# Optimization experiments

Measured on AMD Instinct MI355X. Metric: run time of the kernel, lower is better.

The kernel has to match this reference:

```python
import jax, jax.numpy as jnp
from jax import lax
import numpy as np

H = 512       # nhidden
IN = 300      # title/body input dim
TLEN = 40     # title_len
BLEN = 200    # body_len
B = 256       # batch
CH = 512      # classify_hidden
NC = 4        # nclass


def setup_inputs():
    key = jax.random.key(0)
    ks = jax.random.split(key, 17)
    s = 1.0 / np.sqrt(H)
    u = lambda k, sh: jax.random.uniform(k, sh, jnp.float32, -s, s)
    return {
        "x": jax.random.normal(ks[0], (B, TLEN + BLEN, IN), jnp.float32),
        "title_Wih": u(ks[1], (2, 4 * H, IN)),
        "title_Whh": u(ks[2], (2, 4 * H, H)),
        "title_bih": u(ks[3], (2, 4 * H)),
        "title_bhh": u(ks[4], (2, 4 * H)),
        "body_Wih": u(ks[5], (2, 4 * H, IN)),
        "body_Whh": u(ks[6], (2, 4 * H, H)),
        "body_bih": u(ks[7], (2, 4 * H)),
        "body_bhh": u(ks[8], (2, 4 * H)),
        "bil_W": u(ks[9], (1, 2 * H, 2 * H)),
        "bil_b": u(ks[10], (1,)),
        "attn_W": u(ks[11], (2 * H, 4 * H)),
        "attn_b": u(ks[12], (2 * H,)),
        "dec_W": u(ks[13], (CH, 4 * H)),
        "dec_b": u(ks[14], (CH,)),
        "cls_W": u(ks[15], (NC, CH)),
        "cls_b": u(ks[16], (NC,)),
    }


def _lstm_dir(x, Wih, Whh, bih, bhh, h0, c0, reverse):
    # x: [B, T, I]; precompute input-to-gate contributions for all timesteps
    xg = jnp.einsum('bti,gi->btg', x, Wih) + bih + bhh  # [B, T, 4H]

    def step(carry, xg_t):
        h, c = carry
        g = xg_t + h @ Whh.T  # PyTorch gate order: i, f, g, o
        i, f, gg, o = jnp.split(g, 4, axis=-1)
        c = jax.nn.sigmoid(f) * c + jax.nn.sigmoid(i) * jnp.tanh(gg)
        h = jax.nn.sigmoid(o) * jnp.tanh(c)
        return (h, c), h

    (hT, cT), hs = lax.scan(step, (h0, c0), jnp.swapaxes(xg, 0, 1), reverse=reverse)
    return jnp.swapaxes(hs, 0, 1), hT, cT  # outputs aligned to input time order


def _bilstm(x, Wih, Whh, bih, bhh, h0, c0):
    # h0, c0: [2, B, H] (dir 0 = forward, dir 1 = backward)
    out_f, hf, cf = _lstm_dir(x, Wih[0], Whh[0], bih[0], bhh[0], h0[0], c0[0], False)
    out_b, hb, cb = _lstm_dir(x, Wih[1], Whh[1], bih[1], bhh[1], h0[1], c0[1], True)
    out = jnp.concatenate([out_f, out_b], axis=-1)  # [B, T, 2H]
    return out, jnp.stack([hf, hb]), jnp.stack([cf, cb])


def reference(x, title_Wih, title_Whh, title_bih, title_bhh,
              body_Wih, body_Whh, body_bih, body_bhh,
              bil_W, bil_b, attn_W, attn_b, dec_W, dec_b, cls_W, cls_b):
    title, body = x[:, :TLEN, :], x[:, TLEN:, :]
    z = jnp.zeros((2, x.shape[0], H), x.dtype)
    title_out, hn, cn = _bilstm(title, title_Wih, title_Whh, title_bih, title_bhh, z, z)
    # conditional=True: body RNN starts from title final (h, c)
    body_out, _, _ = _bilstm(body, body_Wih, body_Whh, body_bih, body_bhh, hn, cn)
    body_last = body_out[:, -1, :]  # [B, 2H]
    # vectorized bilinear attention over title timesteps (replaces per-t loop)
    scores = jnp.einsum('bte,oeh,bh->bto', title_out, bil_W, body_last) + bil_b
    scores = jax.nn.softmax(scores[..., 0], axis=-1)  # [B, TLEN]
    context = jnp.einsum('bte,bt->be', title_out, scores)  # [B, 2H]
    attn = jnp.tanh(jnp.concatenate([context, body_last], axis=1) @ attn_W.T + attn_b)
    output = jnp.concatenate([title_out[:, -1, :], attn], axis=1)  # [B, 4H]
    class_hidden = output @ dec_W.T + dec_b  # dropout p=0.0 -> identity
    return jax.nn.softmax(class_hidden @ cls_W.T + cls_b, axis=-1)
```

## Files before the change

### kernel.cpp

```cpp
#include <hip/hip_runtime.h>
#include <math.h>

#define HD    512
#define BATCH 256
#define TDIM  240
#define INDIM 300

typedef unsigned short u16;
typedef u16   u16x8 __attribute__((ext_vector_type(8)));
typedef float f32x4 __attribute__((ext_vector_type(4)));

__device__ __forceinline__ u16 bf16_rte(float v) {
    unsigned u = __builtin_bit_cast(unsigned, v);
    unsigned r = (u + 0x7FFFu + ((u >> 16) & 1u)) >> 16;
    return (u16)r;
}

__device__ __forceinline__ void mfma16(f32x4& d, u16x8 a, u16x8 b) {
    asm("v_mfma_f32_16x16x32_bf16 %0, %1, %2, %0" : "+v"(d) : "v"(a), "v"(b));
}

__global__ __launch_bounds__(256) void split_pad(
    const float* __restrict__ src, u16* __restrict__ hi, u16* __restrict__ lo,
    int rows, int kin, int kout)
// ... 4 lines not shown
    int k = (int)(i - (long)r * kout);
    float v = (k < kin) ? src[(long)r * kin + k] : 0.f;
    u16 h = bf16_rte(v);
    float hf = __builtin_bit_cast(float, (unsigned)h << 16);
    hi[i] = h;
    lo[i] = bf16_rte(v - hf);
}

struct SJob { const float* src; u16* hi; u16* lo; int kin; int kout; };
struct SParams { SJob j[12]; long cum[13]; };

__global__ __launch_bounds__(256) void split_all(SParams P)
{
    long gid = (long)blockIdx.x * 256 + threadIdx.x;
    if (gid >= P.cum[12]) return;
    int sgi = 0;
    #pragma unroll
    for (int k = 1; k < 12; ++k) if (gid >= P.cum[k]) sgi = k;
    const SJob& J = P.j[sgi];
    long i = gid - P.cum[sgi];
    int r = (int)(i / J.kout);
    int k = (int)(i - (long)r * J.kout);
    float v = (k < J.kin) ? J.src[(long)r * J.kin + k] : 0.f;
    u16 h = bf16_rte(v);
    float hf = __builtin_bit_cast(float, (unsigned)h << 16);
    J.hi[i] = h;
    J.lo[i] = bf16_rte(v - hf);
}

struct StepDir {
    const u16* Wih_h; const u16* Wih_l;
    const u16* Whh_h; const u16* Whh_l;
    const float* bih; const float* bhh;
    const u16* hh; const u16* hl;
    u16* oh; u16* ol;
    float* c;
    float* ex; long exs;
    int t;
};

__global__ __launch_bounds__(64) void step_mfma(
    const u16* __restrict__ xh, const u16* __restrict__ xl,
    StepDir d0, StepDir d1)
{
    StepDir D = blockIdx.z ? d1 : d0;
    const int gx   = blockIdx.x;
    const int xcd  = gx & 7, j = gx >> 3;
    const int cblk = xcd * 4 + (j & 3);
    const int rblk = j >> 2;
    const int lane = threadIdx.x;
    const int lr   = lane & 15;
    const int lk8  = (lane >> 4) * 8;
    const int b0   = rblk * 32;
    const int col  = cblk * 16 + lr;

    f32x4 acc[2][4];
    #pragma unroll
    for (int g = 0; g < 4; ++g) {
        float bs = D.bih[g * HD + col] + D.bhh[g * HD + col];
        acc[0][g] = f32x4{bs, bs, bs, bs};
        acc[1][g] = f32x4{bs, bs, bs, bs};
    }

    u16x8 Ah0[2], Al0[2], Bh0[4], Bl0[4];
    u16x8 Ah1[2], Al1[2], Bh1[4], Bl1[4];

    auto MMA = [&](u16x8 (&Ah)[2], u16x8 (&Al)[2], u16x8 (&Bh)[4], u16x8 (&Bl)[4]) {
        #pragma unroll
        for (int rt = 0; rt < 2; ++rt)
            #pragma unroll
            for (int g = 0; g < 4; ++g) {
                mfma16(acc[rt][g], Ah[rt], Bh[g]);
                mfma16(acc[rt][g], Ah[rt], Bl[g]);
                mfma16(acc[rt][g], Al[rt], Bh[g]);
            }
    };

    {
        auto LD = [&](u16x8 (&Ah)[2], u16x8 (&Al)[2], u16x8 (&Bh)[4], u16x8 (&Bl)[4], int ks) {
            const int ko = ks * 32 + lk8;
            #pragma unroll
            for (int rt = 0; rt < 2; ++rt) {
                long off = ((long)(b0 + rt * 16 + lr) * TDIM + D.t) * 320 + ko;
                Ah[rt] = *(const u16x8*)(xh + off);
                Al[rt] = *(const u16x8*)(xl + off);
            }
            #pragma unroll
            for (int g = 0; g < 4; ++g) {
                long off = (long)(g * HD + col) * 320 + ko;
                Bh[g] = *(const u16x8*)(D.Wih_h + off);
                Bl[g] = *(const u16x8*)(D.Wih_l + off);
            }
        };
        LD(Ah0, Al0, Bh0, Bl0, 0);
        #pragma unroll
        for (int ks = 0; ks < 10; ks += 2) {
            LD(Ah1, Al1, Bh1, Bl1, ks + 1);
            MMA(Ah0, Al0, Bh0, Bl0);
            if (ks + 2 < 10) LD(Ah0, Al0, Bh0, Bl0, ks + 2);
            MMA(Ah1, Al1, Bh1, Bl1);
        }
    }
    {
        auto LD = [&](u16x8 (&Ah)[2], u16x8 (&Al)[2], u16x8 (&Bh)[4], u16x8 (&Bl)[4], int ks) {
            const int ko = ks * 32 + lk8;
            #pragma unroll
            for (int rt = 0; rt < 2; ++rt) {
                long off = (long)(b0 + rt * 16 + lr) * HD + ko;
                Ah[rt] = *(const u16x8*)(D.hh + off);
                Al[rt] = *(const u16x8*)(D.hl + off);
            }
            #pragma unroll
            for (int g = 0; g < 4; ++g) {
                long off = (long)(g * HD + col) * HD + ko;
                Bh[g] = *(const u16x8*)(D.Whh_h + off);
                Bl[g] = *(const u16x8*)(D.Whh_l + off);
            }
        };
        LD(Ah0, Al0, Bh0, Bl0, 0);
        #pragma unroll
        for (int ks = 0; ks < 16; ks += 2) {
            LD(Ah1, Al1, Bh1, Bl1, ks + 1);
            MMA(Ah0, Al0, Bh0, Bl0);
            if (ks + 2 < 16) LD(Ah0, Al0, Bh0, Bl0, ks + 2);
            MMA(Ah1, Al1, Bh1, Bl1);
        }
    }

    #pragma unroll
    for (int rt = 0; rt < 2; ++rt) {
        #pragma unroll
        for (int r = 0; r < 4; ++r) {
            const int b = b0 + rt * 16 + (lane >> 4) * 4 + r;
            const long hoff = (long)b * HD + col;
            float iv = acc[rt][0][r];
            float fv = acc[rt][1][r];
            float gv = acc[rt][2][r];
            float ov = acc[rt][3][r];
            float cp = D.c[hoff];
            float si = 1.f / (1.f + expf(-iv));
            float sf = 1.f / (1.f + expf(-fv));
            float so = 1.f / (1.f + expf(-ov));
            float cn = sf * cp + si * tanhf(gv);
            float hn = so * tanhf(cn);
            D.c[hoff] = cn;
            u16 hb = bf16_rte(hn);
            D.oh[hoff] = hb;
            D.ol[hoff] = bf16_rte(hn - __builtin_bit_cast(float, (unsigned)hb << 16));
            if (D.ex) D.ex[(long)b * D.exs + col] = hn;
        }
    }
}

__global__ __launch_bounds__(64) void xg_mfma(
    const u16* __restrict__ xh, const u16* __restrict__ xl,
    const u16* __restrict__ Wih_h, const u16* __restrict__ Wih_l,
    const float* __restrict__ bih, const float* __restrict__ bhh,
    float* __restrict__ xgT, int t0abs, int tstep)
{
    const int bx   = blockIdx.x;
    const int tloc = bx >> 9;
    const int rem  = bx & 511;
    const int rblk = rem >> 6;
    const int cgrp = rem & 63;
    const int lane = threadIdx.x;
    const int lr = lane & 15, lk8 = (lane >> 4) * 8;
    const int b0 = rblk * 32;
    const int tx = t0abs + tstep * tloc;
    const int colf0 = cgrp * 32 + lr;
    const int colf1 = colf0 + 16;

    f32x4 acc[2][2];
    {
        float bs0 = bih[colf0] + bhh[colf0];
        float bs1 = bih[colf1] + bhh[colf1];
        acc[0][0] = f32x4{bs0, bs0, bs0, bs0};
        acc[1][0] = f32x4{bs0, bs0, bs0, bs0};
        acc[0][1] = f32x4{bs1, bs1, bs1, bs1};
        acc[1][1] = f32x4{bs1, bs1, bs1, bs1};
    }

    u16x8 a0h[2], a0l[2], b0h[2], b0l[2];
    u16x8 a1h[2], a1l[2], b1h[2], b1l[2];

    auto LD = [&](u16x8 (&Ah)[2], u16x8 (&Al)[2], u16x8 (&Bh)[2], u16x8 (&Bl)[2], int ks) {
        const int ko = ks * 32 + lk8;
        #pragma unroll
        for (int rt = 0; rt < 2; ++rt) {
            long off = ((long)(b0 + rt * 16 + lr) * TDIM + tx) * 320 + ko;
            Ah[rt] = *(const u16x8*)(xh + off);
            Al[rt] = *(const u16x8*)(xl + off);
        }
        long w0 = (long)colf0 * 320 + ko;
        long w1 = (long)colf1 * 320 + ko;
        Bh[0] = *(const u16x8*)(Wih_h + w0);
        Bl[0] = *(const u16x8*)(Wih_l + w0);
        Bh[1] = *(const u16x8*)(Wih_h + w1);
        Bl[1] = *(const u16x8*)(Wih_l + w1);
    };
    auto MMA = [&](u16x8 (&Ah)[2], u16x8 (&Al)[2], u16x8 (&Bh)[2], u16x8 (&Bl)[2]) {
        #pragma unroll
        for (int rt = 0; rt < 2; ++rt)
            #pragma unroll
            for (int cf = 0; cf < 2; ++cf) {
                mfma16(acc[rt][cf], Ah[rt], Bh[cf]);
                mfma16(acc[rt][cf], Ah[rt], Bl[cf]);
                mfma16(acc[rt][cf], Al[rt], Bh[cf]);
            }
    };

    LD(a0h, a0l, b0h, b0l, 0);
    #pragma unroll
    for (int ks = 0; ks < 10; ks += 2) {
        LD(a1h, a1l, b1h, b1l, ks + 1);
        MMA(a0h, a0l, b0h, b0l);
        if (ks + 2 < 10) LD(a0h, a0l, b0h, b0l, ks + 2);
        MMA(a1h, a1l, b1h, b1l);
    }

    #pragma unroll
    for (int rt = 0; rt < 2; ++rt) {
        long o0 = ((long)tloc * 2048 + colf0) * 256 + b0 + rt * 16 + (lane >> 4) * 4;
        long o1 = ((long)tloc * 2048 + colf1) * 256 + b0 + rt * 16 + (lane >> 4) * 4;
        *(f32x4*)(xgT + o0) = acc[rt][0];
        *(f32x4*)(xgT + o1) = acc[rt][1];
    }
}

__device__ __forceinline__ void group_bar(unsigned* cnt, unsigned* gen,
                                          unsigned nb, unsigned g)
{
    __syncthreads();
    if (threadIdx.x == 0) {
        unsigned old = __hip_atomic_fetch_add(cnt, 1u, __ATOMIC_RELEASE,
                                              __HIP_MEMORY_SCOPE_AGENT);
        if (old == nb - 1u) {
            __hip_atomic_store(cnt, 0u, __ATOMIC_RELAXED, __HIP_MEMORY_SCOPE_AGENT);
            __hip_atomic_store(gen, g + 1u, __ATOMIC_RELEASE, __HIP_MEMORY_SCOPE_AGENT);
        } else {
            while (__hip_atomic_load(gen, __ATOMIC_RELAXED, __HIP_MEMORY_SCOPE_AGENT) < g + 1u)
                __builtin_amdgcn_s_sleep(2);
            (void)__hip_atomic_load(gen, __ATOMIC_ACQUIRE, __HIP_MEMORY_SCOPE_AGENT);
        }
    }
    __syncthreads();
}

__global__ __launch_bounds__(256) void lstm_persist(
    const float* __restrict__ xgT,
    const u16* __restrict__ Whh_h, const u16* __restrict__ Whh_l,
    u16* __restrict__ hAh, u16* __restrict__ hAl,
    u16* __restrict__ hBh, u16* __restrict__ hBl,
    float* __restrict__ cst,
    float* __restrict__ ex, long ex_bstride, int ex_t0, int ex_tstep,
    int ex_coff, int ex_final,
    unsigned* __restrict__ bars, int s0, int L)
{
    const int gx   = blockIdx.x;
    const int rblk = gx & 7;
    const int cblk = gx >> 3;
    const int wid  = threadIdx.x >> 6;
    const int lane = threadIdx.x & 63;
    const int lr   = lane & 15;
    const int lk8  = (lane >> 4) * 8;
    const int b0   = rblk * 32;
    const int col  = cblk * 16 + lr;

    __shared__ u16 WH[64][520];
    __shared__ u16 WL[64][520];
    __shared__ f32x4 RED[3][64][8];

    for (int idx = threadIdx.x; idx < 64 * 64; idx += 256) {
        int rr = idx >> 6;
        int kk = (idx & 63) << 3;
        int g = rr >> 4, cc = rr & 15;
        long gro = (long)(g * HD + cblk * 16 + cc) * HD + kk;
        *(u16x8*)&WH[rr][kk] = *(const u16x8*)(Whh_h + gro);
        *(u16x8*)&WL[rr][kk] = *(const u16x8*)(Whh_l + gro);
    }
    __syncthreads();

    unsigned* bcnt = bars + rblk * 64;
    unsigned* bgen = bars + 512 + rblk * 64;
    unsigned gen = 0;
    const int ksbase = wid * 4;

    for (int ti = 0; ti < L; ++ti) {
        const int s = s0 + ti;
        const u16* hih = (s & 1) ? hBh : hAh;
        const u16* hil = (s & 1) ? hBl : hAl;
        u16* hoh = (s & 1) ? hAh : hBh;
        u16* hol = (s & 1) ? hAl : hBl;

        f32x4 acc[2][4];
        if (wid == 0) {
            #pragma unroll
            for (int rt = 0; rt < 2; ++rt)
                #pragma unroll
                for (int g = 0; g < 4; ++g) {
                    long o = ((long)ti * 2048 + g * HD + col) * 256
                             + b0 + rt * 16 + (lane >> 4) * 4;
                    acc[rt][g] = __builtin_nontemporal_load((const f32x4*)(xgT + o));
                }
        } else {
            #pragma unroll
            for (int rt = 0; rt < 2; ++rt)
                #pragma unroll
                for (int g = 0; g < 4; ++g) acc[rt][g] = f32x4{0.f, 0.f, 0.f, 0.f};
        }

        u16x8 Ah0[2], Al0[2], Bh0[4], Bl0[4];
        u16x8 Ah1[2], Al1[2], Bh1[4], Bl1[4];

        auto MMA = [&](u16x8 (&Ah)[2], u16x8 (&Al)[2], u16x8 (&Bh)[4], u16x8 (&Bl)[4]) {
            #pragma unroll
            for (int rt = 0; rt < 2; ++rt)
                #pragma unroll
                for (int g = 0; g < 4; ++g) {
                    mfma16(acc[rt][g], Ah[rt], Bh[g]);
                    mfma16(acc[rt][g], Ah[rt], Bl[g]);
                    mfma16(acc[rt][g], Al[rt], Bh[g]);
                }
        };
        auto LD = [&](u16x8 (&Ah)[2], u16x8 (&Al)[2], u16x8 (&Bh)[4], u16x8 (&Bl)[4], int ks) {
            const int ko = ks * 32 + lk8;
            #pragma unroll
            for (int rt = 0; rt < 2; ++rt) {
                long off = (long)(b0 + rt * 16 + lr) * HD + ko;
                Ah[rt] = *(const u16x8*)(hih + off);
                Al[rt] = *(const u16x8*)(hil + off);
            }
            #pragma unroll
            for (int g = 0; g < 4; ++g) {
                Bh[g] = *(const u16x8*)&WH[g * 16 + lr][ko];
                Bl[g] = *(const u16x8*)&WL[g * 16 + lr][ko];
            }
        };

        LD(Ah0, Al0, Bh0, Bl0, ksbase + 0);
        LD(Ah1, Al1, Bh1, Bl1, ksbase + 1);
        MMA(Ah0, Al0, Bh0, Bl0);
        LD(Ah0, Al0, Bh0, Bl0, ksbase + 2);
        MMA(Ah1, Al1, Bh1, Bl1);
        LD(Ah1, Al1, Bh1, Bl1, ksbase + 3);
        MMA(Ah0, Al0, Bh0, Bl0);
        MMA(Ah1, Al1, Bh1, Bl1);

        if (wid != 0) {
            #pragma unroll
            for (int rt = 0; rt < 2; ++rt)
                #pragma unroll
                for (int g = 0; g < 4; ++g)
                    RED[wid - 1][lane][rt * 4 + g] = acc[rt][g];
        }
        __syncthreads();

        if (wid == 0) {
            #pragma unroll
            for (int w = 0; w < 3; ++w)
                #pragma unroll
                for (int rt = 0; rt < 2; ++rt)
                    #pragma unroll
                    for (int g = 0; g < 4; ++g)
                        acc[rt][g] += RED[w][lane][rt * 4 + g];

            const bool exw = (ex_final == -2) || (ex_final >= 0 && ti == ex_final);
            const int tt = ex_t0 + ex_tstep * ti;
            #pragma unroll
            for (int rt = 0; rt < 2; ++rt) {
                #pragma unroll
                for (int r = 0; r < 4; ++r) {
                    const int b = b0 + rt * 16 + (lane >> 4) * 4 + r;
                    const long hoff = (long)b * HD + col;
                    float iv = acc[rt][0][r];
                    float fv = acc[rt][1][r];
                    float gv = acc[rt][2][r];
                    float ov = acc[rt][3][r];
                    float cp = cst[hoff];
                    float si = 1.f / (1.f + expf(-iv));
                    float sf = 1.f / (1.f + expf(-fv));
                    float so = 1.f / (1.f + expf(-ov));
                    float cn = sf * cp + si * tanhf(gv);
                    float hn = so * tanhf(cn);
                    cst[hoff] = cn;
                    u16 hb = bf16_rte(hn);
                    hoh[hoff] = hb;
                    hol[hoff] = bf16_rte(hn - __builtin_bit_cast(float, (unsigned)hb << 16));
                    if (exw) ex[(long)b * ex_bstride + (long)tt * 1024 + ex_coff + col] = hn;
                }
            }
        }
        if (ti + 1 < L) { group_bar(bcnt, bgen, 32u, gen); ++gen; }
    }
}

struct DualDir {
    const u16* Whh_h; const u16* Whh_l;
    u16 *hAh, *hAl, *hBh, *hBl;
    float* cst;
    float* ex; long exb; int ext0, extstep, excoff;
};

__global__ __launch_bounds__(256) void lstm_persist_dual(
    const float* __restrict__ xgT, long dirStride,
    DualDir d0, DualDir d1,
    unsigned* __restrict__ bars, int s0, int L)
{
    const int gx   = blockIdx.x;
    const int grp  = gx & 7;
    const int dir  = grp >> 2;
    const int rb2  = grp & 3;
    const int cblk = gx >> 3;
    const int wid  = threadIdx.x >> 6;
    const int lane = threadIdx.x & 63;
    const int lr   = lane & 15;
    const int lk8  = (lane >> 4) * 8;
    const int col  = cblk * 16 + lr;

    const DualDir D = dir ? d1 : d0;
    const float* xgD = xgT + (dir ? dirStride : 0);

    __shared__ u16 WH[64][520];
    __shared__ u16 WL[64][520];
    __shared__ f32x4 RED[3][64][8];

    for (int idx = threadIdx.x; idx < 64 * 64; idx += 256) {
        int rr = idx >> 6;
        int kk = (idx & 63) << 3;
        int g = rr >> 4, cc = rr & 15;
        long gro = (long)(g * HD + cblk * 16 + cc) * HD + kk;
        *(u16x8*)&WH[rr][kk] = *(const u16x8*)(D.Whh_h + gro);
        *(u16x8*)&WL[rr][kk] = *(const u16x8*)(D.Whh_l + gro);
    }
    __syncthreads();

    unsigned* bcnt = bars + grp * 64;
    unsigned* bgen = bars + 512 + grp * 64;
    unsigned gen = 0;
    const int ksbase = wid * 4;

    for (int ti = 0; ti < L; ++ti) {
        const int s = s0 + ti;
        const u16* hih = (s & 1) ? D.hBh : D.hAh;
        const u16* hil = (s & 1) ? D.hBl : D.hAl;
        u16* hoh = (s & 1) ? D.hAh : D.hBh;
        u16* hol = (s & 1) ? D.hAl : D.hBl;

        #pragma unroll
        for (int t2 = 0; t2 < 2; ++t2) {
            const int b0 = rb2 * 64 + t2 * 32;

            f32x4 acc[2][4];
            if (wid == 0) {
                #pragma unroll
                for (int rt = 0; rt < 2; ++rt)
                    #pragma unroll
                    for (int g = 0; g < 4; ++g) {
                        long o = ((long)ti * 2048 + g * HD + col) * 256
                                 + b0 + rt * 16 + (lane >> 4) * 4;
                        acc[rt][g] = __builtin_nontemporal_load((const f32x4*)(xgD + o));
                    }
            } else {
                #pragma unroll
                for (int rt = 0; rt < 2; ++rt)
                    #pragma unroll
                    for (int g = 0; g < 4; ++g) acc[rt][g] = f32x4{0.f, 0.f, 0.f, 0.f};
            }

            u16x8 Ah0[2], Al0[2], Bh0[4], Bl0[4];
            u16x8 Ah1[2], Al1[2], Bh1[4], Bl1[4];

            auto MMA = [&](u16x8 (&Ah)[2], u16x8 (&Al)[2], u16x8 (&Bh)[4], u16x8 (&Bl)[4]) {
                #pragma unroll
                for (int rt = 0; rt < 2; ++rt)
                    #pragma unroll
                    for (int g = 0; g < 4; ++g) {
                        mfma16(acc[rt][g], Ah[rt], Bh[g]);
                        mfma16(acc[rt][g], Ah[rt], Bl[g]);
                        mfma16(acc[rt][g], Al[rt], Bh[g]);
                    }
            };
            auto LD = [&](u16x8 (&Ah)[2], u16x8 (&Al)[2], u16x8 (&Bh)[4], u16x8 (&Bl)[4], int ks) {
                const int ko = ks * 32 + lk8;
                #pragma unroll
                for (int rt = 0; rt < 2; ++rt) {
                    long off = (long)(b0 + rt * 16 + lr) * HD + ko;
                    Ah[rt] = *(const u16x8*)(hih + off);
                    Al[rt] = *(const u16x8*)(hil + off);
                }
                #pragma unroll
                for (int g = 0; g < 4; ++g) {
                    Bh[g] = *(const u16x8*)&WH[g * 16 + lr][ko];
                    Bl[g] = *(const u16x8*)&WL[g * 16 + lr][ko];
                }
            };

            LD(Ah0, Al0, Bh0, Bl0, ksbase + 0);
            LD(Ah1, Al1, Bh1, Bl1, ksbase + 1);
            MMA(Ah0, Al0, Bh0, Bl0);
            LD(Ah0, Al0, Bh0, Bl0, ksbase + 2);
            MMA(Ah1, Al1, Bh1, Bl1);
            LD(Ah1, Al1, Bh1, Bl1, ksbase + 3);
            MMA(Ah0, Al0, Bh0, Bl0);
            MMA(Ah1, Al1, Bh1, Bl1);

            if (wid != 0) {
                #pragma unroll
                for (int rt = 0; rt < 2; ++rt)
                    #pragma unroll
                    for (int g = 0; g < 4; ++g)
                        RED[wid - 1][lane][rt * 4 + g] = acc[rt][g];
            }
            __syncthreads();

            if (wid == 0) {
                #pragma unroll
                for (int w = 0; w < 3; ++w)
                    #pragma unroll
                    for (int rt = 0; rt < 2; ++rt)
                        #pragma unroll
                        for (int g = 0; g < 4; ++g)
                            acc[rt][g] += RED[w][lane][rt * 4 + g];

                const int tt = D.ext0 + D.extstep * ti;
                #pragma unroll
                for (int rt = 0; rt < 2; ++rt) {
                    #pragma unroll
                    for (int r = 0; r < 4; ++r) {
                        const int b = b0 + rt * 16 + (lane >> 4) * 4 + r;
                        const long hoff = (long)b * HD + col;
                        float iv = acc[rt][0][r];
                        float fv = acc[rt][1][r];
                        float gv = acc[rt][2][r];
                        float ov = acc[rt][3][r];
                        float cp = D.cst[hoff];
                        float si = 1.f / (1.f + expf(-iv));
                        float sf = 1.f / (1.f + expf(-fv));
                        float so = 1.f / (1.f + expf(-ov));
                        float cn = sf * cp + si * tanhf(gv);
                        float hn = so * tanhf(cn);
                        D.cst[hoff] = cn;
                        u16 hb = bf16_rte(hn);
                        hoh[hoff] = hb;
                        hol[hoff] = bf16_rte(hn - __builtin_bit_cast(float, (unsigned)hb << 16));
                        D.ex[(long)b * D.exb + (long)tt * 1024 + D.excoff + col] = hn;
                    }
                }
            }
            __syncthreads();
        }
        if (ti + 1 < L) { group_bar(bcnt, bgen, 32u, gen); ++gen; }
    }
}

__global__ __launch_bounds__(64) void body_persist(
    const u16* __restrict__ xh, const u16* __restrict__ xl,
    const u16* __restrict__ Wih_h, const u16* __restrict__ Wih_l,
    const u16* __restrict__ Whh_h, const u16* __restrict__ Whh_l,
    const float* __restrict__ bih, const float* __restrict__ bhh,
    u16* __restrict__ hAh, u16* __restrict__ hAl,
    u16* __restrict__ hBh, u16* __restrict__ hBl,
// ... 353 lines not shown
        }
        __syncthreads();
    }
    #pragma unroll
    for (int r = 0; r < 2; ++r) {
        int m = mblk*32 + ty*2 + r;
        #pragma unroll
        for (int q = 0; q < 4; ++q) {
            int n = nblk*64 + q*16 + txd;
            float v = acc[r][q] + (bias ? bias[n] : 0.f);
            if (ACT == 1) v = tanhf(v);
            C[m*ldc + n] = v;
        }
    }
}

__global__ __launch_bounds__(256) void attn_ctx(
    const float* __restrict__ title_out,
    const float* __restrict__ u,
    const float* __restrict__ bilb,
    float* __restrict__ attn_in)
{
    int b = blockIdx.x;
    int tid = threadIdx.x;
    __shared__ float uL[1024];
    __shared__ float sc[40];
    for (int e = tid; e < 1024; e += 256) uL[e] = u[b*1024 + e];
    __syncthreads();
    int wave = tid >> 6, lane = tid & 63;
    for (int t = wave*10; t < wave*10 + 10; ++t) {
        const float* row = title_out + (b*40 + t)*1024;
        float s = 0.f;
        for (int e = lane; e < 1024; e += 64) s += row[e]*uL[e];
        #pragma unroll
        for (int off = 32; off > 0; off >>= 1) s += __shfl_down(s, off, 64);
        if (lane == 0) sc[t] = s + bilb[0];
    }
    __syncthreads();
    if (tid < 64) {
        float v = (tid < 40) ? sc[tid] : -1e30f;
        float m = v;
        #pragma unroll
        for (int off = 32; off > 0; off >>= 1) m = fmaxf(m, __shfl_xor(m, off, 64));
        float e = (tid < 40) ? expf(v - m) : 0.f;
        float ssum = e;
        #pragma unroll
        for (int off = 32; off > 0; off >>= 1) ssum += __shfl_xor(ssum, off, 64);
        if (tid < 40) sc[tid] = e / ssum;
    }
    __syncthreads();
    for (int e = tid; e < 1024; e += 256) {
        float a = 0.f;
        #pragma unroll
        for (int t = 0; t < 40; ++t) a += sc[t]*title_out[(b*40 + t)*1024 + e];
        attn_in[b*2048 + e] = a;
    }
}

__global__ void copy_rows(const float* __restrict__ src, int ss,
                          float* __restrict__ dst, int ds, int n)
{
    int b = blockIdx.x;
    for (int e = threadIdx.x; e < n; e += blockDim.x) dst[b*ds + e] = src[b*ss + e];
}

__global__ __launch_bounds__(64) void final_cls(
    const float* __restrict__ ch,
    const float* __restrict__ clsW,
    const float* __restrict__ clsb,
    float* __restrict__ out)
{
    int b = blockIdx.x*64 + threadIdx.x;
    float o[4];
    #pragma unroll
    for (int n = 0; n < 4; ++n) {
        float s = clsb[n];
        for (int jj = 0; jj < 512; ++jj) s += ch[b*512 + jj]*clsW[n*512 + jj];
        o[n] = s;
    }
    float m = fmaxf(fmaxf(o[0], o[1]), fmaxf(o[2], o[3]));
    float e0 = expf(o[0]-m), e1 = expf(o[1]-m), e2 = expf(o[2]-m), e3 = expf(o[3]-m);
    float s = e0 + e1 + e2 + e3;
    out[b*4+0] = e0/s; out[b*4+1] = e1/s; out[b*4+2] = e2/s; out[b*4+3] = e3/s;
}

extern "C" void kernel_launch(void* const* d_in, const int* in_sizes, int n_in,
                              void* d_out, int out_size, void* d_ws, size_t ws_size,
                              hipStream_t stream) {
    const float* x     = (const float*)d_in[0];
    const float* tWih  = (const float*)d_in[1];
    const float* tWhh  = (const float*)d_in[2];
    const float* tbih  = (const float*)d_in[3];
    const float* tbhh  = (const float*)d_in[4];
    const float* bWih  = (const float*)d_in[5];
    const float* bWhh  = (const float*)d_in[6];
    const float* bbih  = (const float*)d_in[7];
    const float* bbhh  = (const float*)d_in[8];
    const float* bilW  = (const float*)d_in[9];
    const float* bilb  = (const float*)d_in[10];
    const float* attnW = (const float*)d_in[11];
    const float* attnb = (const float*)d_in[12];
    const float* decW  = (const float*)d_in[13];
    const float* decb  = (const float*)d_in[14];
    const float* clsW  = (const float*)d_in[15];
    const float* clsb  = (const float*)d_in[16];

    char* base = (char*)d_ws;
    size_t off = 0;
    auto carve = [&](size_t bytes) -> void* {
        void* r = base + off; off += (bytes + 255) & ~(size_t)255; return r;
    };

    u16* hA0h = (u16*)carve(BATCH*HD*2);
    u16* hA0l = (u16*)carve(BATCH*HD*2);
    u16* hA1h = (u16*)carve(BATCH*HD*2);
    u16* hA1l = (u16*)carve(BATCH*HD*2);
    float* c0 = (float*)carve(BATCH*HD*4);
    float* c1 = (float*)carve(BATCH*HD*4);
    unsigned* bars = (unsigned*)carve(32*4096);
    size_t zero_bytes = off;
    u16* hB0h = (u16*)carve(BATCH*HD*2);
    u16* hB0l = (u16*)carve(BATCH*HD*2);
    u16* hB1h = (u16*)carve(BATCH*HD*2);
    u16* hB1l = (u16*)carve(BATCH*HD*2);
    u16* xh = (u16*)carve((size_t)BATCH*TDIM*320*2);
    u16* xl = (u16*)carve((size_t)BATCH*TDIM*320*2);
    u16* tW0ih_h = (u16*)carve(2048*320*2); u16* tW0ih_l = (u16*)carve(2048*320*2);
    u16* tW1ih_h = (u16*)carve(2048*320*2); u16* tW1ih_l = (u16*)carve(2048*320*2);
    u16* bW0ih_h = (u16*)carve(2048*320*2); u16* bW0ih_l = (u16*)carve(2048*320*2);
    u16* bW1ih_h = (u16*)carve(2048*320*2); u16* bW1ih_l = (u16*)carve(2048*320*2);
    u16* tW0hh_h = (u16*)carve(2048*512*2); u16* tW0hh_l = (u16*)carve(2048*512*2);
    u16* tW1hh_h = (u16*)carve(2048*512*2); u16* tW1hh_l = (u16*)carve(2048*512*2);
    u16* bW0hh_h = (u16*)carve(2048*512*2); u16* bW0hh_l = (u16*)carve(2048*512*2);
    u16* bW1hh_h = (u16*)carve(2048*512*2); u16* bW1hh_l = (u16*)carve(2048*512*2);
    float* title_out = (float*)carve((size_t)BATCH*40*1024*4);
    float* body_last = (float*)carve((size_t)BATCH*1024*4);
    float* u_buf     = (float*)carve((size_t)BATCH*1024*4);
    float* attn_in   = (float*)carve((size_t)BATCH*2048*4);
    float* out_cat   = (float*)carve((size_t)BATCH*2048*4);
    float* ch        = (float*)carve((size_t)BATCH*512*4);
    u16* bl_h = (u16*)carve((size_t)BATCH*1024*2); u16* bl_l = (u16*)carve((size_t)BATCH*1024*2);
    u16* ai_h = (u16*)carve((size_t)BATCH*2048*2); u16* ai_l = (u16*)carve((size_t)BATCH*2048*2);
    u16* oc_h = (u16*)carve((size_t)BATCH*2048*2); u16* oc_l = (u16*)carve((size_t)BATCH*2048*2);
    u16* bilW_h  = (u16*)carve(1024*1024*2); u16* bilW_l  = (u16*)carve(1024*1024*2);
    u16* attnW_h = (u16*)carve((size_t)1024*2048*2); u16* attnW_l = (u16*)carve((size_t)1024*2048*2);
    u16* decW_h  = (u16*)carve((size_t)512*2048*2);  u16* decW_l  = (u16*)carve((size_t)512*2048*2);
    size_t need = off;

    const size_t SLAB_BYTES = (size_t)2048 * 256 * 4;
    const long   SLABF = 2048L * 256;
    float* xgT = (float*)(base + off);
    size_t nslab = 0;
    if (ws_size > need) nslab = (ws_size - need) / SLAB_BYTES;
    int C = (int)(nslab > 50 ? 50 : nslab);
    const bool xg_ok = (C >= 10);
    int C2 = (int)(nslab / 2 > 40 ? 40 : nslab / 2);
    const bool dual_ok = (C2 >= 10);

    if (ws_size >= need) {
        hipMemsetAsync(d_ws, 0, zero_bytes, stream);

        {
            SParams P;
            auto J = [&](int i, const float* s, u16* h, u16* l, long rows, int kin, int kout) {
                P.j[i] = { s, h, l, kin, kout };
                P.cum[i + 1] = P.cum[i] + rows * (long)kout;
            };
            P.cum[0] = 0;
            J(0,  x,                  xh,      xl,      (long)BATCH*TDIM, INDIM, 320);
            J(1,  tWih,               tW0ih_h, tW0ih_l, 2048, INDIM, 320);
            J(2,  tWih + 2048*INDIM,  tW1ih_h, tW1ih_l, 2048, INDIM, 320);
            J(3,  bWih,               bW0ih_h, bW0ih_l, 2048, INDIM, 320);
            J(4,  bWih + 2048*INDIM,  bW1ih_h, bW1ih_l, 2048, INDIM, 320);
            J(5,  tWhh,               tW0hh_h, tW0hh_l, 2048, HD, HD);
            J(6,  tWhh + 2048*HD,     tW1hh_h, tW1hh_l, 2048, HD, HD);
            J(7,  bWhh,               bW0hh_h, bW0hh_l, 2048, HD, HD);
            J(8,  bWhh + 2048*HD,     bW1hh_h, bW1hh_l, 2048, HD, HD);
            J(9,  bilW,               bilW_h,  bilW_l,  1024, 1024, 1024);
            J(10, attnW,              attnW_h, attnW_l, 1024, 2048, 2048);
            J(11, decW,               decW_h,  decW_l,  512,  2048, 2048);
            long total = P.cum[12];
            split_all<<<dim3((unsigned)((total + 255) / 256)), 256, 0, stream>>>(P);
        }

        if (xg_ok) {
            int ci = 0;
            if (dual_ok) {
                for (int tb = 0; tb < 40; tb += C2, ++ci) {
                    int L = (C2 < 40 - tb) ? C2 : (40 - tb);
                    xg_mfma<<<dim3((unsigned)(L*512)), 64, 0, stream>>>(
                        xh, xl, tW0ih_h, tW0ih_l, tbih, tbhh, xgT, tb, 1);
                    xg_mfma<<<dim3((unsigned)(L*512)), 64, 0, stream>>>(
                        xh, xl, tW1ih_h, tW1ih_l, tbih + 2048, tbhh + 2048,
                        xgT + (long)L * SLABF, 39 - tb, -1);
                    DualDir D0 = { tW0hh_h, tW0hh_l, hA0h, hA0l, hB0h, hB0l, c0,
                                   title_out, 40*1024, tb, 1, 0 };
                    DualDir D1 = { tW1hh_h, tW1hh_l, hA1h, hA1l, hB1h, hB1l, c1,
                                   title_out, 40*1024, 39 - tb, -1, 512 };
                    lstm_persist_dual<<<dim3(256), 256, 0, stream>>>(
                        xgT, (long)L * SLABF, D0, D1,
                        bars + (size_t)ci*1024, tb, L);
                }
            } else {
                for (int tb = 0; tb < 40; tb += C, ++ci) {
                    int L = (C < 40 - tb) ? C : (40 - tb);
                    xg_mfma<<<dim3((unsigned)(L*512)), 64, 0, stream>>>(
                        xh, xl, tW0ih_h, tW0ih_l, tbih, tbhh, xgT, tb, 1);
                    lstm_persist<<<dim3(256), 256, 0, stream>>>(
                        xgT, tW0hh_h, tW0hh_l, hA0h, hA0l, hB0h, hB0l, c0,
                        title_out, 40*1024, tb, 1, 0, -2,
                        bars + (size_t)ci*1024, tb, L);
                }
                for (int tb = 0; tb < 40; tb += C, ++ci) {
                    int L = (C < 40 - tb) ? C : (40 - tb);
                    xg_mfma<<<dim3((unsigned)(L*512)), 64, 0, stream>>>(
                        xh, xl, tW1ih_h, tW1ih_l, tbih + 2048, tbhh + 2048, xgT, 39 - tb, -1);
                    lstm_persist<<<dim3(256), 256, 0, stream>>>(
                        xgT, tW1hh_h, tW1hh_l, hA1h, hA1l, hB1h, hB1l, c1,
                        title_out, 40*1024, 39 - tb, -1, 512, -2,
                        bars + (size_t)ci*1024, tb, L);
                }
            }
            {
                StepDir F = { bW0ih_h, bW0ih_l, bW0hh_h, bW0hh_l, bbih, bbhh,
                              hA0h, hA0l, hB0h, hB0l, c0, (float*)nullptr, 0, 40 };
                StepDir R = { bW1ih_h, bW1ih_l, bW1hh_h, bW1hh_l, bbih + 2048, bbhh + 2048,
                              hA1h, hA1l, hB1h, hB1l, c1, body_last + 512, 1024, 239 };
                step_mfma<<<dim3(256,1,2), 64, 0, stream>>>(xh, xl, F, R);
            }
            for (int tb = 1; tb < 200; tb += C, ++ci) {
                int L = (C < 200 - tb) ? C : (200 - tb);
                bool last = (tb + L == 200);
                xg_mfma<<<dim3((unsigned)(L*512)), 64, 0, stream>>>(
                    xh, xl, bW0ih_h, bW0ih_l, bbih, bbhh, xgT, 40 + tb, 1);
                lstm_persist<<<dim3(256), 256, 0, stream>>>(
                    xgT, bW0hh_h, bW0hh_l, hA0h, hA0l, hB0h, hB0l, c0,
                    body_last, 1024, 0, 0, 0, last ? (L - 1) : -1,
                    bars + (size_t)ci*1024, 40 + tb, L);
            }
        } else {
            for (int t = 0; t < 40; ++t) {
                bool odd = t & 1;
                StepDir A = { tW0ih_h, tW0ih_l, tW0hh_h, tW0hh_l, tbih, tbhh,
                              odd?hB0h:hA0h, odd?hB0l:hA0l, odd?hA0h:hB0h, odd?hA0l:hB0l,
                              c0, title_out + (size_t)t*1024, 40*1024, t };
                StepDir B = { tW1ih_h, tW1ih_l, tW1hh_h, tW1hh_l, tbih + 2048, tbhh + 2048,
                              odd?hB1h:hA1h, odd?hB1l:hA1l, odd?hA1h:hB1h, odd?hA1l:hB1l,
                              c1, title_out + (size_t)(39 - t)*1024 + 512, 40*1024, 39 - t };
                step_mfma<<<dim3(256,1,2), 64, 0, stream>>>(xh, xl, A, B);
            }
            {
                StepDir F = { bW0ih_h, bW0ih_l, bW0hh_h, bW0hh_l, bbih, bbhh,
                              hA0h, hA0l, hB0h, hB0l, c0, (float*)nullptr, 0, 40 };
                StepDir R = { bW1ih_h, bW1ih_l, bW1hh_h, bW1hh_l, bbih + 2048, bbhh + 2048,
                              hA1h, hA1l, hB1h, hB1l, c1, body_last + 512, 1024, 239 };
                step_mfma<<<dim3(256,1,2), 64, 0, stream>>>(xh, xl, F, R);
            }
            body_persist<<<dim3(256), 64, 0, stream>>>(
                xh, xl, bW0ih_h, bW0ih_l, bW0hh_h, bW0hh_l, bbih, bbhh,
                hA0h, hA0l, hB0h, hB0l, c0, body_last, bars);
        }

        split_pad<<<dim3((unsigned)((256*1024 + 255)/256)), 256, 0, stream>>>(
            body_last, bl_h, bl_l, 256, 1024, 1024);
        mfma_gemm<0><<<dim3(8*64), 64, 0, stream>>>(bl_h, bl_l, bilW_h, bilW_l,
                                                    (const float*)nullptr, u_buf, 1024, 1024, 64);
        attn_ctx<<<256, 256, 0, stream>>>(title_out, u_buf, bilb, attn_in);
        copy_rows<<<256, 256, 0, stream>>>(body_last, 1024, attn_in + 1024, 2048, 1024);
        copy_rows<<<256, 256, 0, stream>>>(title_out + 39*1024, 40*1024, out_cat, 2048, 1024);
        split_pad<<<dim3((unsigned)((256*2048 + 255)/256)), 256, 0, stream>>>(
            attn_in, ai_h, ai_l, 256, 2048, 2048);
        mfma_gemm<1><<<dim3(8*64), 64, 0, stream>>>(ai_h, ai_l, attnW_h, attnW_l,
                                                    attnb, out_cat + 1024, 2048, 2048, 64);
        split_pad<<<dim3((unsigned)((256*2048 + 255)/256)), 256, 0, stream>>>(
            out_cat, oc_h, oc_l, 256, 2048, 2048);
        mfma_gemm<0><<<dim3(8*32), 64, 0, stream>>>(oc_h, oc_l, decW_h, decW_l,
                                                    decb, ch, 512, 2048, 32);
        final_cls<<<4, 64, 0, stream>>>(ch, clsW, clsb, (float*)d_out);
    } else {
        float* p = (float*)d_ws;
        float* lhA0 = p; p += BATCH*HD;
        float* lc0  = p; p += BATCH*HD;
        float* lhA1 = p; p += BATCH*HD;
        float* lc1  = p; p += BATCH*HD;
        float* lhB0 = p; p += BATCH*HD;
        float* lhB1 = p; p += BATCH*HD;
        float* l_title = p; p += (size_t)BATCH*40*1024;
        float* l_blast = p; p += BATCH*1024;
        float* l_u     = p; p += BATCH*1024;
        float* l_ain   = p; p += BATCH*2048;
        float* l_ocat  = p; p += BATCH*2048;
        float* l_ch    = p; p += BATCH*512;

        hipMemsetAsync(lhA0, 0, (size_t)4*BATCH*HD*sizeof(float), stream);
        const float* tWih1 = tWih + 2048*INDIM;
        const float* tWhh1 = tWhh + 2048*HD;
        const float* bWih1 = bWih + 2048*INDIM;
        const float* bWhh1 = bWhh + 2048*HD;

        for (int t = 0; t < 40; ++t) {
            float* hi0 = (t & 1) ? lhB0 : lhA0;
            float* ho0 = (t & 1) ? lhA0 : lhB0;
            float* hi1 = (t & 1) ? lhB1 : lhA1;
            float* ho1 = (t & 1) ? lhA1 : lhB1;
            lstm_step<64><<<dim3(4,32,2), 256, 0, stream>>>(
                x, tWih, tWhh, tbih, tbhh, hi0, ho0, lc0,
                l_title + t*1024, 40*1024, t,
                tWih1, tWhh1, tbih + 2048, tbhh + 2048, hi1, ho1, lc1,
                l_title + (39 - t)*1024 + 512, 40*1024, 39 - t);
        }
        lstm_step<64><<<dim3(4,32,2), 256, 0, stream>>>(
            x, bWih, bWhh, bbih, bbhh, lhA0, lhB0, lc0, (float*)nullptr, 0, 40,
            bWih1, bWhh1, bbih + 2048, bbhh + 2048, lhA1, lhB1, lc1, l_blast + 512, 1024, 239);
        for (int t = 1; t < 200; ++t) {
            int s = 40 + t;
            float* hi = (s & 1) ? lhB0 : lhA0;
            float* ho = (s & 1) ? lhA0 : lhB0;
            float* exp_ = (t == 199) ? l_blast : (float*)nullptr;
            lstm_step<32><<<dim3(8,32,1), 256, 0, stream>>>(
                x, bWih, bWhh, bbih, bbhh, hi, ho, lc0, exp_, 1024, 40 + t,
                nullptr, nullptr, nullptr, nullptr, nullptr, nullptr, nullptr,
                (float*)nullptr, 0, 0);
        }
        gemm_bias_act<0><<<dim3(8,16), 256, 0, stream>>>(l_blast, 1024, bilW, nullptr, l_u, 1024, 1024);
        attn_ctx<<<256, 256, 0, stream>>>(l_title, l_u, bilb, l_ain);
        copy_rows<<<256, 256, 0, stream>>>(l_blast, 1024, l_ain + 1024, 2048, 1024);
        copy_rows<<<256, 256, 0, stream>>>(l_title + 39*1024, 40*1024, l_ocat, 2048, 1024);
        gemm_bias_act<1><<<dim3(8,16), 256, 0, stream>>>(l_ain, 2048, attnW, attnb, l_ocat + 1024, 2048, 2048);
        gemm_bias_act<0><<<dim3(8,8), 256, 0, stream>>>(l_ocat, 2048, decW, decb, l_ch, 512, 2048);
        final_cls<<<4, 64, 0, stream>>>(l_ch, clsW, clsb, (float*)d_out);
    }
}
```

Before: 4.798 ms.

## Overlap next-chunk input projection with persistent LSTM recurrence via extra blocks

The input-projection GEMM is refactored into a device function. The persistent LSTM kernels (single and dual direction) get extra blocks beyond the first 256, and those blocks compute the xg projection for the next body chunk into a double-buffered slab. This removes the separate xg_mfma launches between body chunks and aims to hide projection work behind the serial recurrence. The trade-off is more workspace for two body buffers, which may shrink chunk size C and add chunks and barriers. Also, because the kernel's large static LDS is reserved for every block, the extra blocks may not fit alongside the recurrence blocks and could simply run after them.

```diff
diff --git a/kernel.cpp b/kernel.cpp
--- a/kernel.cpp
+++ b/kernel.cpp
@@ -180,18 +180,17 @@
     }
 }
 
-__global__ __launch_bounds__(64) void xg_mfma(
+__device__ __forceinline__ void xg_job(
+    int bx, int lane,
     const u16* __restrict__ xh, const u16* __restrict__ xl,
     const u16* __restrict__ Wih_h, const u16* __restrict__ Wih_l,
     const float* __restrict__ bih, const float* __restrict__ bhh,
     float* __restrict__ xgT, int t0abs, int tstep)
 {
-    const int bx   = blockIdx.x;
     const int tloc = bx >> 9;
     const int rem  = bx & 511;
     const int rblk = rem >> 6;
     const int cgrp = rem & 63;
-    const int lane = threadIdx.x;
     const int lr = lane & 15, lk8 = (lane >> 4) * 8;
     const int b0 = rblk * 32;
     const int tx = t0abs + tstep * tloc;
@@ -254,6 +253,21 @@
         *(f32x4*)(xgT + o1) = acc[rt][1];
     }
 }
+
+__global__ __launch_bounds__(64) void xg_mfma(
+    const u16* __restrict__ xh, const u16* __restrict__ xl,
+    const u16* __restrict__ Wih_h, const u16* __restrict__ Wih_l,
+    const float* __restrict__ bih, const float* __restrict__ bhh,
+    float* __restrict__ xgT, int t0abs, int tstep)
+{
+    xg_job(blockIdx.x, threadIdx.x, xh, xl, Wih_h, Wih_l, bih, bhh, xgT, t0abs, tstep);
+}
+
+struct NextXG {
+    const u16* Wih_h; const u16* Wih_l;
+    const float* bih; const float* bhh;
+    float* dst; int t0abs; int tstep; int L;
+};
 
 __device__ __forceinline__ void group_bar(unsigned* cnt, unsigned* gen,
                                           unsigned nb, unsigned g)
@@ -282,9 +296,20 @@
     float* __restrict__ cst,
     float* __restrict__ ex, long ex_bstride, int ex_t0, int ex_tstep,
     int ex_coff, int ex_final,
-    unsigned* __restrict__ bars, int s0, int L)
-{
-    const int gx   = blockIdx.x;
+    unsigned* __restrict__ bars, int s0, int L,
+    const u16* __restrict__ xh, const u16* __restrict__ xl, NextXG nx)
+{
+    const int gx = blockIdx.x;
+    if (gx >= 256) {
+        const long Jtot = (long)nx.L * 512;
+        const int pw = threadIdx.x >> 6, pl = threadIdx.x & 63;
+        const long stride = ((long)gridDim.x - 256) * 4;
+        for (long j = ((long)gx - 256) * 4 + pw; j < Jtot; j += stride)
+            xg_job((int)j, pl, xh, xl, nx.Wih_h, nx.Wih_l, nx.bih, nx.bhh,
+                   nx.dst, nx.t0abs, nx.tstep);
+        return;
+    }
+
     const int rblk = gx & 7;
     const int cblk = gx >> 3;
     const int wid  = threadIdx.x >> 6;
@@ -432,9 +457,20 @@
 __global__ __launch_bounds__(256) void lstm_persist_dual(
     const float* __restrict__ xgT, long dirStride,
     DualDir d0, DualDir d1,
-    unsigned* __restrict__ bars, int s0, int L)
-{
-    const int gx   = blockIdx.x;
+    unsigned* __restrict__ bars, int s0, int L,
+    const u16* __restrict__ xh, const u16* __restrict__ xl, NextXG nx)
+{
+    const int gx = blockIdx.x;
+    if (gx >= 256) {
+        const long Jtot = (long)nx.L * 512;
+        const int pw = threadIdx.x >> 6, pl = threadIdx.x & 63;
+        const long stride = ((long)gridDim.x - 256) * 4;
+        for (long j = ((long)gx - 256) * 4 + pw; j < Jtot; j += stride)
+            xg_job((int)j, pl, xh, xl, nx.Wih_h, nx.Wih_l, nx.bih, nx.bhh,
+                   nx.dst, nx.t0abs, nx.tstep);
+        return;
+    }
+
     const int grp  = gx & 7;
     const int dir  = grp >> 2;
     const int rb2  = grp & 3;
@@ -1094,10 +1130,17 @@
     float* xgT = (float*)(base + off);
     size_t nslab = 0;
     if (ws_size > need) nslab = (ws_size - need) / SLAB_BYTES;
-    int C = (int)(nslab > 50 ? 50 : nslab);
-    const bool xg_ok = (C >= 10);
+
     int C2 = (int)(nslab / 2 > 40 ? 40 : nslab / 2);
     const bool dual_ok = (C2 >= 10);
+    long rem = dual_ok ? ((long)nslab - 2 * C2) : (long)nslab;
+    bool overlap = dual_ok && (rem >= 20);
+    int C = overlap ? (int)(rem / 2 > 50 ? 50 : rem / 2)
+                    : (int)(nslab > 50 ? 50 : nslab);
+    const bool xg_ok = (C >= 10);
+    float* bodyA = overlap ? (xgT + (long)2 * C2 * SLABF) : xgT;
+    float* bodyB = overlap ? (bodyA + (long)C * SLABF) : xgT;
+    auto bodyBuf = [&](int k) { return (k & 1) ? bodyB : bodyA; };
 
     if (ws_size >= need) {
         hipMemsetAsync(d_ws, 0, zero_bytes, stream);
@@ -1125,10 +1168,22 @@
             split_all<<<dim3((unsigned)((total + 255) / 256)), 256, 0, stream>>>(P);
         }
 
+        const NextXG nxNone = { nullptr, nullptr, nullptr, nullptr, nullptr, 0, 0, 0 };
+
         if (xg_ok) {
             int ci = 0;
+            int bodyTb[8], bodyL[8], nbody = 0;
+            for (int tb = 1; tb < 200; tb += C) {
+                bodyTb[nbody] = tb;
+                bodyL[nbody] = (C < 200 - tb) ? C : (200 - tb);
+                ++nbody;
+            }
+
             if (dual_ok) {
-                for (int tb = 0; tb < 40; tb += C2, ++ci) {
+                int ntc = 0;
+                for (int tb = 0; tb < 40; tb += C2) ++ntc;
+                int tc = 0;
+                for (int tb = 0; tb < 40; tb += C2, ++ci, ++tc) {
                     int L = (C2 < 40 - tb) ? C2 : (40 - tb);
                     xg_mfma<<<dim3((unsigned)(L*512)), 64, 0, stream>>>(
                         xh, xl, tW0ih_h, tW0ih_l, tbih, tbhh, xgT, tb, 1);
@@ -1139,9 +1194,16 @@
                                    title_out, 40*1024, tb, 1, 0 };
                     DualDir D1 = { tW1hh_h, tW1hh_l, hA1h, hA1l, hB1h, hB1l, c1,
                                    title_out, 40*1024, 39 - tb, -1, 512 };
-                    lstm_persist_dual<<<dim3(256), 256, 0, stream>>>(
+                    NextXG nx = nxNone;
+                    unsigned nxb = 0;
+                    if (overlap && tc == ntc - 1 && nbody > 0) {
+                        nx = { bW0ih_h, bW0ih_l, bbih, bbhh, bodyBuf(0),
+                               40 + bodyTb[0], 1, bodyL[0] };
+                        nxb = (unsigned)(((long)bodyL[0] * 512 + 3) / 4);
+                    }
+                    lstm_persist_dual<<<dim3(256 + nxb), 256, 0, stream>>>(
                         xgT, (long)L * SLABF, D0, D1,
-                        bars + (size_t)ci*1024, tb, L);
+                        bars + (size_t)ci*1024, tb, L, xh, xl, nx);
                 }
             } else {
                 for (int tb = 0; tb < 40; tb += C, ++ci) {
@@ -1151,7 +1213,7 @@
                     lstm_persist<<<dim3(256), 256, 0, stream>>>(
                         xgT, tW0hh_h, tW0hh_l, hA0h, hA0l, hB0h, hB0l, c0,
                         title_out, 40*1024, tb, 1, 0, -2,
-                        bars + (size_t)ci*1024, tb, L);
+                        bars + (size_t)ci*1024, tb, L, xh, xl, nxNone);
                 }
                 for (int tb = 0; tb < 40; tb += C, ++ci) {
                     int L = (C < 40 - tb) ? C : (40 - tb);
@@ -1160,7 +1222,7 @@
                     lstm_persist<<<dim3(256), 256, 0, stream>>>(
                         xgT, tW1hh_h, tW1hh_l, hA1h, hA1l, hB1h, hB1l, c1,
                         title_out, 40*1024, 39 - tb, -1, 512, -2,
-                        bars + (size_t)ci*1024, tb, L);
+                        bars + (size_t)ci*1024, tb, L, xh, xl, nxNone);
                 }
             }
             {
@@ -1170,15 +1232,30 @@
                               hA1h, hA1l, hB1h, hB1l, c1, body_last + 512, 1024, 239 };
                 step_mfma<<<dim3(256,1,2), 64, 0, stream>>>(xh, xl, F, R);
             }
-            for (int tb = 1; tb < 200; tb += C, ++ci) {
-                int L = (C < 200 - tb) ? C : (200 - tb);
+            for (int k = 0; k < nbody; ++k, ++ci) {
+                int tb = bodyTb[k], L = bodyL[k];
                 bool last = (tb + L == 200);
-                xg_mfma<<<dim3((unsigned)(L*512)), 64, 0, stream>>>(
-                    xh, xl, bW0ih_h, bW0ih_l, bbih, bbhh, xgT, 40 + tb, 1);
-                lstm_persist<<<dim3(256), 256, 0, stream>>>(
-                    xgT, bW0hh_h, bW0hh_l, hA0h, hA0l, hB0h, hB0l, c0,
+                float* buf;
+                if (overlap) {
+                    buf = bodyBuf(k);
+                    if (!(k == 0)) {  }
+                    else {  }
+                } else {
+                    buf = xgT;
+                    xg_mfma<<<dim3((unsigned)(L*512)), 64, 0, stream>>>(
+                        xh, xl, bW0ih_h, bW0ih_l, bbih, bbhh, buf, 40 + tb, 1);
+                }
+                NextXG nx = nxNone;
+                unsigned nxb = 0;
+                if (overlap && k + 1 < nbody) {
+                    nx = { bW0ih_h, bW0ih_l, bbih, bbhh, bodyBuf(k + 1),
+                           40 + bodyTb[k + 1], 1, bodyL[k + 1] };
+                    nxb = (unsigned)(((long)bodyL[k + 1] * 512 + 3) / 4);
+                }
+                lstm_persist<<<dim3(256 + nxb), 256, 0, stream>>>(
+                    buf, bW0hh_h, bW0hh_l, hA0h, hA0l, hB0h, hB0l, c0,
                     body_last, 1024, 0, 0, 0, last ? (L - 1) : -1,
-                    bars + (size_t)ci*1024, 40 + tb, L);
+                    bars + (size_t)ci*1024, 40 + tb, L, xh, xl, nx);
             }
         } else {
             for (int t = 0; t < 40; ++t) {
```

Measured after the change: 4.802 ms. Within noise of the previous version (+0.1%).
